# Performance work log

Measured on AMD Instinct MI355X. Metric: run time of the kernel, lower is better.

Reference implementation:

```python
import jax, jax.numpy as jnp
import numpy as np

B, C, P, D = 4096, 1000, 10, 256
N = C * P            # total prototypes
E = 160000           # edges among prototypes
MARGIN = -0.1
LOSS_WEIGHT = 0.1
EPS = 1e-12          # F.normalize eps


def _gcn_conv(x, src, dst, deg_isqrt, w, b):
    # PyG GCNConv: symmetric-normalized aggregation with self-loops (added by caller)
    xw = x @ w                                   # [N, D]
    norm = deg_isqrt[src] * deg_isqrt[dst]       # [E+N]
    msg = norm[:, None] * xw[src]                # [E+N, D]
    out = jax.ops.segment_sum(msg, dst, num_segments=N)
    return out + b


def setup_inputs() -> dict:
    key = jax.random.key(0)
    ks = jax.random.split(key, 8)
    return {
        "hidden": jax.random.normal(ks[0], (B, D), jnp.float32),
        "labels": jax.random.randint(ks[1], (B,), 0, C),
        "edge_index": jax.random.randint(ks[2], (2, E), 0, N),
        "node_features": 0.02 * jax.random.normal(ks[3], (N, D), jnp.float32),
        "w1": jax.random.normal(ks[4], (D, D), jnp.float32) / np.sqrt(D),
        "b1": jnp.zeros((D,), jnp.float32),
        "w2": jax.random.normal(ks[5], (D, D), jnp.float32) / np.sqrt(D),
        "b2": jnp.zeros((D,), jnp.float32),
    }


def reference(hidden, labels, edge_index, node_features, w1, b1, w2, b2):
    # --- PrototypeGCN over the prototype graph (self-loops + sym norm) ---
    loops = jnp.arange(N, dtype=edge_index.dtype)
    src = jnp.concatenate([edge_index[0], loops])
    dst = jnp.concatenate([edge_index[1], loops])
    deg = jax.ops.segment_sum(jnp.ones_like(dst, jnp.float32), dst, num_segments=N)
    deg_isqrt = jnp.where(deg > 0, jax.lax.rsqrt(jnp.maximum(deg, 1.0)), 0.0)
    x = node_features
    x = jax.nn.relu(_gcn_conv(x, src, dst, deg_isqrt, w1, b1))
    x = jax.nn.relu(_gcn_conv(x, src, dst, deg_isqrt, w2, b2))

    # --- cosine similarity, per-class max over prototypes ---
    hidden_norm = hidden / jnp.maximum(jnp.linalg.norm(hidden, axis=1, keepdims=True), EPS)
    proto_norm = x / jnp.maximum(jnp.linalg.norm(x, axis=1, keepdims=True), EPS)
    sim = (1.0 + hidden_norm @ proto_norm.T) / 2.0          # [B, N]
    sim_pc = sim.reshape(B, C, P)
    output = sim_pc.max(axis=2)                              # [B, C]
    topk_idx = sim_pc.argmax(axis=2)                         # [B, C]

    # --- margin-masked cross entropy ---
    ar = jnp.arange(B)
    true_scores = output[ar, labels]
    pred_labels = output.argmax(axis=1)
    pred_scores = output.max(axis=1)
    mask = (true_scores - pred_scores) > MARGIN              # [B] bool
    cnt = mask.sum()
    per_ce = -jax.nn.log_softmax(output, axis=1)[ar, labels]
    ce_loss = jnp.sum(per_ce * mask) / jnp.maximum(cnt, 1).astype(per_ce.dtype)

    # dispersion = -mean(proto_norm @ proto_norm.T) = -||sum_i p_i||^2 / N^2
    s = proto_norm.sum(axis=0)
    dispersion_loss = -(s @ s) / (N * N)
    total_loss = jnp.where(cnt == 0, 0.0, ce_loss + LOSS_WEIGHT * dispersion_loss)

    # --- vectorized usage scatter (replaces Python double loop) ---
    pos_ids = labels * P + topk_idx[ar, labels]
    positive_usage = jnp.zeros((N,), jnp.float32).at[pos_ids].add(1.0)
    wrong = (pred_labels != labels).astype(jnp.float32)
    neg_ids = pred_labels * P + topk_idx[ar, pred_labels]
    negative_usage = jnp.zeros((N,), jnp.float32).at[neg_ids].add(wrong)

    return (output, total_loss, positive_usage, negative_usage)
```

## Files before the change

### kernel.cpp

```cpp
#include <hip/hip_runtime.h>
#include <math.h>

#define B_  4096
#define C_  1000
#define P_  10
#define D_  256
#define N_  10000
#define E_  160000

typedef __attribute__((ext_vector_type(8))) short short8;
typedef __attribute__((ext_vector_type(4))) float floatx4;

#define MFMA16(a, b, c) __builtin_amdgcn_mfma_f32_16x16x32_bf16((a), (b), (c), 0, 0, 0)

__device__ __forceinline__ float waveReduceSum(float v){
  #pragma unroll
  for (int o = 32; o > 0; o >>= 1) v += __shfl_xor(v, o);
  return v;
}
__device__ __forceinline__ unsigned short f2bf(float f){
  unsigned int u = __float_as_uint(f);
  unsigned int r = (u + 0x7FFFu + ((u >> 16) & 1u)) >> 16;
  return (unsigned short)r;
}
__device__ __forceinline__ float bf2f(unsigned short b){
  return __uint_as_float(((unsigned int)b) << 16);
}
__device__ __forceinline__ void gload_lds16(const void* g, void* l){
  __builtin_amdgcn_global_load_lds((const __attribute__((address_space(1))) void*)g,
                                   (__attribute__((address_space(3))) void*)l, 16, 0, 0);
}
__device__ __forceinline__ void split8(const float* __restrict__ p, short8& h8, short8& l8){
  float4 v0 = *(const float4*)p;
  float4 v1 = *(const float4*)(p + 4);
  float v[8] = {v0.x, v0.y, v0.z, v0.w, v1.x, v1.y, v1.z, v1.w};
  #pragma unroll
  for (int j = 0; j < 8; ++j){
    unsigned short h = f2bf(v[j]);
    h8[j] = (short)h;
    l8[j] = (short)f2bf(v[j] - bf2f(h));
  }
}

__global__ void k_scatter(const int* __restrict__ src, const int* __restrict__ dst,
                          int* __restrict__ cursor, int* __restrict__ csr_src){
  int e = blockIdx.x * 256 + threadIdx.x;
  if (e >= E_) return;
  int d = dst[e];
  int p = atomicAdd(&cursor[d], 1);
  p = (p < 63) ? p : 63;
  csr_src[d * 64 + p] = src[e];
}

__global__ void k_isq(const int* __restrict__ deg, float* __restrict__ isq){
  int n = blockIdx.x * 256 + threadIdx.x;
  if (n < N_) isq[n] = 1.0f / sqrtf((float)(deg[n] + 1));
}

__global__ void k_split_w(const float* __restrict__ w1, const float* __restrict__ w2,
                          unsigned short* __restrict__ w1h, unsigned short* __restrict__ w1l,
                          unsigned short* __restrict__ w2h, unsigned short* __restrict__ w2l){
  int b = blockIdx.x;
  int k = threadIdx.x;
  const float* w = (b < 256) ? w1 : w2;
  int n = b & 255;
  float x = w[(size_t)k * 256 + n];
  unsigned short h = f2bf(x);
  unsigned short l = f2bf(x - bf2f(h));
  if (b < 256){ w1h[(size_t)n * 256 + k] = h; w1l[(size_t)n * 256 + k] = l; }
  else        { w2h[(size_t)n * 256 + k] = h; w2l[(size_t)n * 256 + k] = l; }
}

__global__ __launch_bounds__(64) void k_gemm_mfma(
    const float* __restrict__ A,
    const unsigned short* __restrict__ Wh, const unsigned short* __restrict__ Wl,
    float* __restrict__ outp){
  int lane = threadIdx.x;
  int l15 = lane & 15, lq = lane >> 4;
  int rb = blockIdx.x * 64;
  int nb = blockIdx.y * 32;

  floatx4 acc[4][2];
  #pragma unroll
  for (int mt = 0; mt < 4; ++mt)
    #pragma unroll
    for (int nt = 0; nt < 2; ++nt) acc[mt][nt] = (floatx4){0.f,0.f,0.f,0.f};

  int arow[4];
  #pragma unroll
  for (int mt = 0; mt < 4; ++mt){
    int r = rb + mt * 16 + l15;
    arow[mt] = (r < N_) ? r : (N_ - 1);
  }
  for (int kc = 0; kc < 256; kc += 32){
    short8 ah[4], al[4], bh[2], bl[2];
    #pragma unroll
    for (int mt = 0; mt < 4; ++mt)
      split8(A + (size_t)arow[mt] * 256 + kc + lq * 8, ah[mt], al[mt]);
    #pragma unroll
    for (int nt = 0; nt < 2; ++nt){
      size_t o = (size_t)(nb + nt * 16 + l15) * 256 + kc + lq * 8;
      bh[nt] = *(const short8*)(Wh + o);
      bl[nt] = *(const short8*)(Wl + o);
    }
    #pragma unroll
    for (int nt = 0; nt < 2; ++nt)
      #pragma unroll
      for (int mt = 0; mt < 4; ++mt) acc[mt][nt] = MFMA16(al[mt], bh[nt], acc[mt][nt]);
    #pragma unroll
    for (int nt = 0; nt < 2; ++nt)
      #pragma unroll
      for (int mt = 0; mt < 4; ++mt) acc[mt][nt] = MFMA16(ah[mt], bl[nt], acc[mt][nt]);
    #pragma unroll
    for (int nt = 0; nt < 2; ++nt)
      #pragma unroll
      for (int mt = 0; mt < 4; ++mt) acc[mt][nt] = MFMA16(ah[mt], bh[nt], acc[mt][nt]);
  }
  #pragma unroll
  for (int mt = 0; mt < 4; ++mt)
    #pragma unroll
    for (int r = 0; r < 4; ++r){
      int row = rb + mt * 16 + lq * 4 + r;
      if (row < N_){
        #pragma unroll
        for (int nt = 0; nt < 2; ++nt)
          outp[(size_t)row * 256 + nb + nt * 16 + l15] = acc[mt][nt][r];
      }
    }
}

__global__ void k_agg_relu(const float* __restrict__ XW, const int* __restrict__ deg,
                           const int* __restrict__ csr_src, const float* __restrict__ isq,
                           const float* __restrict__ bias, float* __restrict__ X1){
  int n    = blockIdx.x * 4 + (threadIdx.x >> 6);
  int lane = threadIdx.x & 63;
  int c4   = lane * 4;
  int dg = deg[n]; dg = (dg < 64) ? dg : 64;
  int   esr = (lane < dg) ? csr_src[n * 64 + lane] : 0;
  float is  = isq[n];
  float en  = isq[esr] * is;
  float4 s = *(const float4*)(XW + (size_t)n * 256 + c4);
  float w = is * is;
  float4 a = make_float4(w * s.x, w * s.y, w * s.z, w * s.w);
  int i = 0;
  for (; i + 3 < dg; i += 4){
    int s0 = __shfl(esr, i),   s1 = __shfl(esr, i+1), s2 = __shfl(esr, i+2), s3 = __shfl(esr, i+3);
    float n0 = __shfl(en, i),  n1 = __shfl(en, i+1),  n2 = __shfl(en, i+2),  n3 = __shfl(en, i+3);
    float4 v0 = *(const float4*)(XW + (size_t)s0 * 256 + c4);
    float4 v1 = *(const float4*)(XW + (size_t)s1 * 256 + c4);
    float4 v2 = *(const float4*)(XW + (size_t)s2 * 256 + c4);
    float4 v3 = *(const float4*)(XW + (size_t)s3 * 256 + c4);
    a.x += n0*v0.x + n1*v1.x + n2*v2.x + n3*v3.x;
    a.y += n0*v0.y + n1*v1.y + n2*v2.y + n3*v3.y;
    a.z += n0*v0.z + n1*v1.z + n2*v2.z + n3*v3.z;
    a.w += n0*v0.w + n1*v1.w + n2*v2.w + n3*v3.w;
  }
  for (; i < dg; ++i){
    int s0 = __shfl(esr, i); float n0 = __shfl(en, i);
    float4 v0 = *(const float4*)(XW + (size_t)s0 * 256 + c4);
    a.x += n0 * v0.x; a.y += n0 * v0.y; a.z += n0 * v0.z; a.w += n0 * v0.w;
  }
  float4 b = *(const float4*)(bias + c4);
  float4 o;
  o.x = fmaxf(a.x + b.x, 0.f); o.y = fmaxf(a.y + b.y, 0.f);
  o.z = fmaxf(a.z + b.z, 0.f); o.w = fmaxf(a.w + b.w, 0.f);
  *(float4*)(X1 + (size_t)n * 256 + c4) = o;
}

__global__ void k_agg_norm_split(const float* __restrict__ XW, const int* __restrict__ deg,
                                 const int* __restrict__ csr_src, const float* __restrict__ isq,
                                 const float* __restrict__ bias,
                                 unsigned short* __restrict__ Ph, unsigned short* __restrict__ Pl){
  int n    = blockIdx.x * 4 + (threadIdx.x >> 6);
  int lane = threadIdx.x & 63;
  int c4   = lane * 4;
  int dg = deg[n]; dg = (dg < 64) ? dg : 64;
  int   esr = (lane < dg) ? csr_src[n * 64 + lane] : 0;
  float is  = isq[n];
  float en  = isq[esr] * is;
  float4 s = *(const float4*)(XW + (size_t)n * 256 + c4);
  float w = is * is;
  float4 a = make_float4(w * s.x, w * s.y, w * s.z, w * s.w);
  int i = 0;
  for (; i + 3 < dg; i += 4){
    int s0 = __shfl(esr, i),   s1 = __shfl(esr, i+1), s2 = __shfl(esr, i+2), s3 = __shfl(esr, i+3);
    float n0 = __shfl(en, i),  n1 = __shfl(en, i+1),  n2 = __shfl(en, i+2),  n3 = __shfl(en, i+3);
    float4 v0 = *(const float4*)(XW + (size_t)s0 * 256 + c4);
    float4 v1 = *(const float4*)(XW + (size_t)s1 * 256 + c4);
    float4 v2 = *(const float4*)(XW + (size_t)s2 * 256 + c4);
    float4 v3 = *(const float4*)(XW + (size_t)s3 * 256 + c4);
    a.x += n0*v0.x + n1*v1.x + n2*v2.x + n3*v3.x;
    a.y += n0*v0.y + n1*v1.y + n2*v2.y + n3*v3.y;
    a.z += n0*v0.z + n1*v1.z + n2*v2.z + n3*v3.z;
    a.w += n0*v0.w + n1*v1.w + n2*v2.w + n3*v3.w;
  }
  for (; i < dg; ++i){
    int s0 = __shfl(esr, i); float n0 = __shfl(en, i);
    float4 v0 = *(const float4*)(XW + (size_t)s0 * 256 + c4);
    a.x += n0 * v0.x; a.y += n0 * v0.y; a.z += n0 * v0.z; a.w += n0 * v0.w;
  }
  float4 b = *(const float4*)(bias + c4);
  float x0 = fmaxf(a.x + b.x, 0.f), x1 = fmaxf(a.y + b.y, 0.f);
  float x2 = fmaxf(a.z + b.z, 0.f), x3 = fmaxf(a.w + b.w, 0.f);
  float ss = x0*x0 + x1*x1 + x2*x2 + x3*x3;
  float tot = waveReduceSum(ss);
  float nrm = fmaxf(sqrtf(tot), 1e-12f);
  x0 /= nrm; x1 /= nrm; x2 /= nrm; x3 /= nrm;
  unsigned short h0 = f2bf(x0), h1 = f2bf(x1), h2 = f2bf(x2), h3 = f2bf(x3);
  ushort4 hv = make_ushort4(h0, h1, h2, h3);
  ushort4 lv = make_ushort4(f2bf(x0 - bf2f(h0)), f2bf(x1 - bf2f(h1)),
                            f2bf(x2 - bf2f(h2)), f2bf(x3 - bf2f(h3)));
  *(ushort4*)(Ph + (size_t)n * 256 + c4) = hv;
  *(ushort4*)(Pl + (size_t)n * 256 + c4) = lv;
}

__global__ void k_norm_split(const float* __restrict__ in,
                             unsigned short* __restrict__ hi,
                             unsigned short* __restrict__ lo){
  int r = blockIdx.x, t = threadIdx.x;
  float v = in[(size_t)r * 256 + t];
  float ss = waveReduceSum(v * v);
  __shared__ float red[4];
  int w = t >> 6;
  if ((t & 63) == 0) red[w] = ss;
  __syncthreads();
  float tot = red[0] + red[1] + red[2] + red[3];
  float nrm = fmaxf(sqrtf(tot), 1e-12f);
  float x = v / nrm;
  unsigned short h = f2bf(x);
  unsigned short l = f2bf(x - bf2f(h));
  hi[(size_t)r * 256 + t] = h;
  lo[(size_t)r * 256 + t] = l;
}

__global__ void k_colsum(const unsigned short* __restrict__ hi,
                         const unsigned short* __restrict__ lo,
                         float* __restrict__ s){
  int d = threadIdx.x;
  int r0 = blockIdx.x * 100;
  float acc = 0.f;
  for (int r = r0; r < r0 + 100; ++r)
    acc += bf2f(hi[(size_t)r * 256 + d]) + bf2f(lo[(size_t)r * 256 + d]);
  atomicAdd(&s[d], acc);
}

__global__ __launch_bounds__(256, 4) void k_sim_max(
    const unsigned short* __restrict__ HNh, const unsigned short* __restrict__ HNl,
    const unsigned short* __restrict__ PNh, const unsigned short* __restrict__ PNl,
    float* __restrict__ out, unsigned char* __restrict__ idxb){
  __shared__ __align__(16) char smem[20736];

  int tid  = threadIdx.x;
  int wid  = tid >> 6;
  int lane = tid & 63;
  int l15  = lane & 15, lq = lane >> 4;
  int rbw  = blockIdx.y * 128 + wid * 32;
  int cb80 = blockIdx.x * 80;

  int swz  = (l15 >> 1) & 3;
  int srow = lane >> 2;
  int skq  = (lane & 3) ^ ((lane >> 3) & 3);

  floatx4 acc[2][5];
  #pragma unroll
  for (int mt = 0; mt < 2; ++mt)
    #pragma unroll
    for (int nt = 0; nt < 5; ++nt) acc[mt][nt] = (floatx4){0.f,0.f,0.f,0.f};

  const unsigned short* a0h = HNh + (size_t)(rbw + l15) * 256 + lq * 8;
  const unsigned short* a0l = HNl + (size_t)(rbw + l15) * 256 + lq * 8;

  auto stage1 = [&](int kc, int pb, int c){
    int bsel = (c >= 5) ? 1 : 0;
    int s = c - bsel * 5;
    int row = s * 16 + srow;
    const unsigned short* gp = (bsel ? PNl : PNh)
        + (size_t)(cb80 + row) * 256 + kc + skq * 8;
    char* lp = smem + pb * 10240 + bsel * 5120 + s * 1024;
    gload_lds16(gp, lp);
  };
  auto stageAll = [&](int kc, int pb){
    stage1(kc, pb, wid);
    stage1(kc, pb, wid + 4);
    if (wid < 2) stage1(kc, pb, wid + 8);
  };

  stageAll(0, 0);
  short8 ah[2], al[2];
  #pragma unroll
  for (int mt = 0; mt < 2; ++mt){
    ah[mt] = *(const short8*)(a0h + (size_t)mt * 4096);
    al[mt] = *(const short8*)(a0l + (size_t)mt * 4096);
  }
  __syncthreads();

  int p = 0;
  for (int kc = 0; kc < 256; kc += 32){
    const unsigned short* Bh = (const unsigned short*)(smem + p * 10240);
    const unsigned short* Bl = Bh + 2560;
    short8 ah2[2], al2[2];
    if (kc < 224){
      stageAll(kc + 32, p ^ 1);
      #pragma unroll
      for (int mt = 0; mt < 2; ++mt){
        ah2[mt] = *(const short8*)(a0h + (size_t)mt * 4096 + kc + 32);
        al2[mt] = *(const short8*)(a0l + (size_t)mt * 4096 + kc + 32);
      }
    }
    #pragma unroll
    for (int nt2 = 0; nt2 < 4; nt2 += 2){
      int ro0 = ((nt2    ) * 16 + l15) * 32 + (lq ^ swz) * 8;
      int ro1 = ((nt2 + 1) * 16 + l15) * 32 + (lq ^ swz) * 8;
      short8 bh0 = *(const short8*)(Bh + ro0), bl0 = *(const short8*)(Bl + ro0);
      short8 bh1 = *(const short8*)(Bh + ro1), bl1 = *(const short8*)(Bl + ro1);
      acc[0][nt2]   = MFMA16(al[0], bh0, acc[0][nt2]);
      acc[1][nt2]   = MFMA16(al[1], bh0, acc[1][nt2]);
      acc[0][nt2+1] = MFMA16(al[0], bh1, acc[0][nt2+1]);
      acc[1][nt2+1] = MFMA16(al[1], bh1, acc[1][nt2+1]);
      acc[0][nt2]   = MFMA16(ah[0], bl0, acc[0][nt2]);
      acc[1][nt2]   = MFMA16(ah[1], bl0, acc[1][nt2]);
      acc[0][nt2+1] = MFMA16(ah[0], bl1, acc[0][nt2+1]);
      acc[1][nt2+1] = MFMA16(ah[1], bl1, acc[1][nt2+1]);
      acc[0][nt2]   = MFMA16(ah[0], bh0, acc[0][nt2]);
      acc[1][nt2]   = MFMA16(ah[1], bh0, acc[1][nt2]);
      acc[0][nt2+1] = MFMA16(ah[0], bh1, acc[0][nt2+1]);
      acc[1][nt2+1] = MFMA16(ah[1], bh1, acc[1][nt2+1]);
    }
    {
      int ro = (4 * 16 + l15) * 32 + (lq ^ swz) * 8;
      short8 bh = *(const short8*)(Bh + ro), bl = *(const short8*)(Bl + ro);
      acc[0][4] = MFMA16(al[0], bh, acc[0][4]);
      acc[1][4] = MFMA16(al[1], bh, acc[1][4]);
      acc[0][4] = MFMA16(ah[0], bl, acc[0][4]);
      acc[1][4] = MFMA16(ah[1], bl, acc[1][4]);
      acc[0][4] = MFMA16(ah[0], bh, acc[0][4]);
      acc[1][4] = MFMA16(ah[1], bh, acc[1][4]);
    }
    ah[0] = ah2[0]; ah[1] = ah2[1];
    al[0] = al2[0]; al[1] = al2[1];
    __syncthreads();
    p ^= 1;
  }

  float* redw = (float*)smem + wid * 1296;
  #pragma unroll
  for (int mt = 0; mt < 2; ++mt){
    #pragma unroll
    for (int nt = 0; nt < 5; ++nt)
      #pragma unroll
      for (int r = 0; r < 4; ++r)
        redw[(lq * 4 + r) * 81 + nt * 16 + l15] = acc[mt][nt][r];
    int row = lane >> 2;
    int q   = lane & 3;
    const float* basep = redw + row * 81 + q * 20;
    float vs[2]; int is[2];
    #pragma unroll
    for (int cc = 0; cc < 2; ++cc){
      float m = 0.5f * (1.0f + basep[cc * 10]); int mi = 0;
      #pragma unroll
      for (int p2 = 1; p2 < 10; ++p2){
        float v = 0.5f * (1.0f + basep[cc * 10 + p2]);
        if (v > m){ m = v; mi = p2; }
      }
      vs[cc] = m; is[cc] = mi;
    }
    int grow = rbw + mt * 16 + row;
    int gcol = blockIdx.x * 8 + q * 2;
    *(float2*)(out + (size_t)grow * 1000 + gcol) = make_float2(vs[0], vs[1]);
    idxb[(size_t)grow * 1000 + gcol]     = (unsigned char)is[0];
    idxb[(size_t)grow * 1000 + gcol + 1] = (unsigned char)is[1];
  }
}

__global__ void k_row_pass(const float* __restrict__ out, const unsigned char* __restrict__ idxb,
                           const int* __restrict__ labels, int* __restrict__ cnt,
                           float* __restrict__ ce_sum, float* __restrict__ pos_usage,
                           float* __restrict__ neg_usage){
  int b = blockIdx.x * 4 + (threadIdx.x >> 6);
  int lane = threadIdx.x & 63;
  const float* row = out + (size_t)b * 1000;
  float m = -INFINITY, s = 0.f; int bi = 0x7fffffff;
  for (int c = lane; c < 1000; c += 64){
    float v = row[c];
    if (v > m){ s = s * expf(m - v) + 1.f; bi = c; m = v; }
    else       s += expf(v - m);
  }
  #pragma unroll
  for (int o = 32; o > 0; o >>= 1){
    float m2 = __shfl_xor(m, o);
    float s2 = __shfl_xor(s, o);
    int   b2 = __shfl_xor(bi, o);
    float M = fmaxf(m, m2);
    s = s * expf(m - M) + s2 * expf(m2 - M);
    if (m2 > m || (m2 == m && b2 < bi)) bi = b2;
    m = M;
  }
  if (lane == 0){
    int lab = labels[b];
    float true_score = row[lab];
    float per_ce = m + logf(s) - true_score;
    bool mask = (true_score - m) > -0.1f;
    if (mask){ atomicAdd(cnt, 1); atomicAdd(ce_sum, per_ce); }
    int pi = idxb[(size_t)b * 1000 + lab];
    atomicAdd(&pos_usage[lab * P_ + pi], 1.f);
    if (bi != lab){
      int ni = idxb[(size_t)b * 1000 + bi];
      atomicAdd(&neg_usage[bi * P_ + ni], 1.f);
    }
  }
}

__global__ void k_finalize(const float* __restrict__ s, const int* __restrict__ cnt,
                           const float* __restrict__ ce_sum, float* __restrict__ loss_out){
  int t = threadIdx.x;
  float v = s[t];
  float ss = waveReduceSum(v * v);
  __shared__ float red[4];
  if ((t & 63) == 0) red[t >> 6] = ss;
  __syncthreads();
  if (t == 0){
    float tot = red[0] + red[1] + red[2] + red[3];
    float disp = -tot / 1.0e8f;
    int c = *cnt;
    float total = (c == 0) ? 0.f
                : (*ce_sum / (float)(c < 1 ? 1 : c) + 0.1f * disp);
    *loss_out = total;
  }
}

extern "C" void kernel_launch(void* const* d_in, const int* in_sizes, int n_in,
                              void* d_out, int out_size, void* d_ws, size_t ws_size,
                              hipStream_t stream){
  const float* hidden = (const float*)d_in[0];
  const int*   labels = (const int*)  d_in[1];
  const int*   eidx   = (const int*)  d_in[2];
  const float* nodef  = (const float*)d_in[3];
  const float* w1     = (const float*)d_in[4];
  const float* b1     = (const float*)d_in[5];
  const float* w2     = (const float*)d_in[6];
  const float* b2     = (const float*)d_in[7];

  float* out       = (float*)d_out;
  float* loss_out  = out + (size_t)B_ * C_;
  float* pos_usage = loss_out + 1;
  float* neg_usage = pos_usage + N_;

  const int* srcp = eidx;
  const int* dstp = eidx + E_;

  char* base = (char*)d_ws;
  size_t off = 0;
  auto alloc = [&](size_t bytes) -> char* {
    char* p = base + off;
    off = (off + bytes + 255) & ~(size_t)255;
    return p;
  };
  int*   cursor  = (int*)  alloc((size_t)N_ * 4);
  float* svec    = (float*)alloc(256 * 4);
  int*   cnt     = (int*)  alloc(4);
  float* ce_sum  = (float*)alloc(4);
  size_t zero_bytes = off;
  float* deg_isqrt = (float*)alloc((size_t)N_ * 4);
  int*   csr_src   = (int*)  alloc((size_t)N_ * 64 * 4);
  float* XW        = (float*)alloc((size_t)N_ * 256 * 4);
  float* X1        = (float*)alloc((size_t)N_ * 256 * 4);
  unsigned short* Ph  = (unsigned short*)alloc((size_t)N_ * 256 * 2);
  unsigned short* Pl  = (unsigned short*)alloc((size_t)N_ * 256 * 2);
  unsigned short* W1h = (unsigned short*)alloc(256 * 256 * 2);
  unsigned short* W1l = (unsigned short*)alloc(256 * 256 * 2);
  unsigned short* W2h = (unsigned short*)alloc(256 * 256 * 2);
  unsigned short* W2l = (unsigned short*)alloc(256 * 256 * 2);
  unsigned short* HNh = (unsigned short*)alloc((size_t)B_ * 256 * 2);
  unsigned short* HNl = (unsigned short*)alloc((size_t)B_ * 256 * 2);
  unsigned char* idxb = (unsigned char*)alloc((size_t)B_ * C_);

  hipMemsetAsync(base, 0, zero_bytes, stream);
  hipMemsetAsync(loss_out, 0, (size_t)(1 + 2 * N_) * 4, stream);

  k_scatter<<<(E_ + 255) / 256, 256, 0, stream>>>(srcp, dstp, cursor, csr_src);
  k_isq<<<(N_ + 255) / 256, 256, 0, stream>>>(cursor, deg_isqrt);
  k_split_w<<<512, 256, 0, stream>>>(w1, w2, W1h, W1l, W2h, W2l);

  dim3 ggrid(157, 8);
  k_gemm_mfma<<<ggrid, 64, 0, stream>>>(nodef, W1h, W1l, XW);
  k_agg_relu<<<N_ / 4, 256, 0, stream>>>(XW, cursor, csr_src, deg_isqrt, b1, X1);
  k_gemm_mfma<<<ggrid, 64, 0, stream>>>(X1, W2h, W2l, XW);
  k_agg_norm_split<<<N_ / 4, 256, 0, stream>>>(XW, cursor, csr_src, deg_isqrt, b2, Ph, Pl);

  k_norm_split<<<B_, 256, 0, stream>>>(hidden, HNh, HNl);
  k_colsum<<<100, 256, 0, stream>>>(Ph, Pl, svec);

  dim3 sgrid(125, 32);
  k_sim_max<<<sgrid, 256, 0, stream>>>(HNh, HNl, Ph, Pl, out, idxb);

  k_row_pass<<<B_ / 4, 256, 0, stream>>>(out, idxb, labels, cnt, ce_sum, pos_usage, neg_usage);
  k_finalize<<<1, 256, 0, stream>>>(svec, cnt, ce_sum, loss_out);
}
```

Measured before the change: 354.7 us.

## Merge prep kernels, inline degree rsqrt, fuse colsum into norm_split

Combines the edge scatter, weight split and output zeroing into one launch, and drops the separate inverse-sqrt-degree kernel by computing it inline from the degree counts in both aggregation kernels. The column-sum kernel is folded into the hidden-normalize launch as extra blocks. It also raises the occupancy hint on the similarity kernel from 4 to 5 blocks per unit. The aim is fewer kernel launches and memsets, at the cost of an extra gathered degree load and a tighter register budget in the similarity kernel.

```diff
diff --git a/kernel.cpp b/kernel.cpp
--- a/kernel.cpp
+++ b/kernel.cpp
@@ -42,33 +42,35 @@
   }
 }
 
-__global__ void k_scatter(const int* __restrict__ src, const int* __restrict__ dst,
-                          int* __restrict__ cursor, int* __restrict__ csr_src){
-  int e = blockIdx.x * 256 + threadIdx.x;
-  if (e >= E_) return;
-  int d = dst[e];
-  int p = atomicAdd(&cursor[d], 1);
-  p = (p < 63) ? p : 63;
-  csr_src[d * 64 + p] = src[e];
-}
-
-__global__ void k_isq(const int* __restrict__ deg, float* __restrict__ isq){
-  int n = blockIdx.x * 256 + threadIdx.x;
-  if (n < N_) isq[n] = 1.0f / sqrtf((float)(deg[n] + 1));
-}
-
-__global__ void k_split_w(const float* __restrict__ w1, const float* __restrict__ w2,
-                          unsigned short* __restrict__ w1h, unsigned short* __restrict__ w1l,
-                          unsigned short* __restrict__ w2h, unsigned short* __restrict__ w2l){
+__global__ void k_prep(const int* __restrict__ src, const int* __restrict__ dst,
+                       int* __restrict__ cursor, int* __restrict__ csr_src,
+                       const float* __restrict__ w1, const float* __restrict__ w2,
+                       unsigned short* __restrict__ w1h, unsigned short* __restrict__ w1l,
+                       unsigned short* __restrict__ w2h, unsigned short* __restrict__ w2l,
+                       float* __restrict__ zero_zone){
   int b = blockIdx.x;
-  int k = threadIdx.x;
-  const float* w = (b < 256) ? w1 : w2;
-  int n = b & 255;
-  float x = w[(size_t)k * 256 + n];
-  unsigned short h = f2bf(x);
-  unsigned short l = f2bf(x - bf2f(h));
-  if (b < 256){ w1h[(size_t)n * 256 + k] = h; w1l[(size_t)n * 256 + k] = l; }
-  else        { w2h[(size_t)n * 256 + k] = h; w2l[(size_t)n * 256 + k] = l; }
+  if (b < 625){
+    int e = b * 256 + threadIdx.x;
+    if (e < E_){
+      int d = dst[e];
+      int p = atomicAdd(&cursor[d], 1);
+      p = (p < 63) ? p : 63;
+      csr_src[d * 64 + p] = src[e];
+    }
+  } else if (b < 1137){
+    int bb = b - 625;
+    int k = threadIdx.x;
+    const float* w = (bb < 256) ? w1 : w2;
+    int n = bb & 255;
+    float x = w[(size_t)k * 256 + n];
+    unsigned short h = f2bf(x);
+    unsigned short l = f2bf(x - bf2f(h));
+    if (bb < 256){ w1h[(size_t)n * 256 + k] = h; w1l[(size_t)n * 256 + k] = l; }
+    else         { w2h[(size_t)n * 256 + k] = h; w2l[(size_t)n * 256 + k] = l; }
+  } else {
+    int i = (b - 1137) * 256 + threadIdx.x;
+    if (i < 1 + 2 * N_) zero_zone[i] = 0.f;
+  }
 }
 
 __global__ __launch_bounds__(64) void k_gemm_mfma(
@@ -130,15 +132,16 @@
 }
 
 __global__ void k_agg_relu(const float* __restrict__ XW, const int* __restrict__ deg,
-                           const int* __restrict__ csr_src, const float* __restrict__ isq,
+                           const int* __restrict__ csr_src,
                            const float* __restrict__ bias, float* __restrict__ X1){
   int n    = blockIdx.x * 4 + (threadIdx.x >> 6);
   int lane = threadIdx.x & 63;
   int c4   = lane * 4;
-  int dg = deg[n]; dg = (dg < 64) ? dg : 64;
+  int dgn = deg[n];
+  int dg = (dgn < 64) ? dgn : 64;
   int   esr = (lane < dg) ? csr_src[n * 64 + lane] : 0;
-  float is  = isq[n];
-  float en  = isq[esr] * is;
+  float is  = 1.0f / sqrtf((float)(dgn + 1));
+  float en  = (1.0f / sqrtf((float)(deg[esr] + 1))) * is;
   float4 s = *(const float4*)(XW + (size_t)n * 256 + c4);
   float w = is * is;
   float4 a = make_float4(w * s.x, w * s.y, w * s.z, w * s.w);
@@ -168,16 +171,17 @@
 }
 
 __global__ void k_agg_norm_split(const float* __restrict__ XW, const int* __restrict__ deg,
-                                 const int* __restrict__ csr_src, const float* __restrict__ isq,
+                                 const int* __restrict__ csr_src,
                                  const float* __restrict__ bias,
                                  unsigned short* __restrict__ Ph, unsigned short* __restrict__ Pl){
   int n    = blockIdx.x * 4 + (threadIdx.x >> 6);
   int lane = threadIdx.x & 63;
   int c4   = lane * 4;
-  int dg = deg[n]; dg = (dg < 64) ? dg : 64;
+  int dgn = deg[n];
+  int dg = (dgn < 64) ? dgn : 64;
   int   esr = (lane < dg) ? csr_src[n * 64 + lane] : 0;
-  float is  = isq[n];
-  float en  = isq[esr] * is;
+  float is  = 1.0f / sqrtf((float)(dgn + 1));
+  float en  = (1.0f / sqrtf((float)(deg[esr] + 1))) * is;
   float4 s = *(const float4*)(XW + (size_t)n * 256 + c4);
   float w = is * is;
   float4 a = make_float4(w * s.x, w * s.y, w * s.z, w * s.w);
@@ -216,35 +220,35 @@
 
 __global__ void k_norm_split(const float* __restrict__ in,
                              unsigned short* __restrict__ hi,
-                             unsigned short* __restrict__ lo){
+                             unsigned short* __restrict__ lo,
+                             const unsigned short* __restrict__ Ph,
+                             const unsigned short* __restrict__ Pl,
+                             float* __restrict__ svec){
   int r = blockIdx.x, t = threadIdx.x;
-  float v = in[(size_t)r * 256 + t];
-  float ss = waveReduceSum(v * v);
-  __shared__ float red[4];
-  int w = t >> 6;
-  if ((t & 63) == 0) red[w] = ss;
-  __syncthreads();
-  float tot = red[0] + red[1] + red[2] + red[3];
-  float nrm = fmaxf(sqrtf(tot), 1e-12f);
-  float x = v / nrm;
-  unsigned short h = f2bf(x);
-  unsigned short l = f2bf(x - bf2f(h));
-  hi[(size_t)r * 256 + t] = h;
-  lo[(size_t)r * 256 + t] = l;
-}
-
-__global__ void k_colsum(const unsigned short* __restrict__ hi,
-                         const unsigned short* __restrict__ lo,
-                         float* __restrict__ s){
-  int d = threadIdx.x;
-  int r0 = blockIdx.x * 100;
-  float acc = 0.f;
-  for (int r = r0; r < r0 + 100; ++r)
-    acc += bf2f(hi[(size_t)r * 256 + d]) + bf2f(lo[(size_t)r * 256 + d]);
-  atomicAdd(&s[d], acc);
-}
-
-__global__ __launch_bounds__(256, 4) void k_sim_max(
+  if (r < B_){
+    float v = in[(size_t)r * 256 + t];
+    float ss = waveReduceSum(v * v);
+    __shared__ float red[4];
+    int w = t >> 6;
+    if ((t & 63) == 0) red[w] = ss;
+    __syncthreads();
+    float tot = red[0] + red[1] + red[2] + red[3];
+    float nrm = fmaxf(sqrtf(tot), 1e-12f);
+    float x = v / nrm;
+    unsigned short h = f2bf(x);
+    unsigned short l = f2bf(x - bf2f(h));
+    hi[(size_t)r * 256 + t] = h;
+    lo[(size_t)r * 256 + t] = l;
+  } else {
+    int r0 = (r - B_) * 100;
+    float acc = 0.f;
+    for (int rr = r0; rr < r0 + 100; ++rr)
+      acc += bf2f(Ph[(size_t)rr * 256 + t]) + bf2f(Pl[(size_t)rr * 256 + t]);
+    atomicAdd(&svec[t], acc);
+  }
+}
+
+__global__ __launch_bounds__(256, 5) void k_sim_max(
     const unsigned short* __restrict__ HNh, const unsigned short* __restrict__ HNl,
     const unsigned short* __restrict__ PNh, const unsigned short* __restrict__ PNl,
     float* __restrict__ out, unsigned char* __restrict__ idxb){
@@ -460,7 +464,6 @@
   int*   cnt     = (int*)  alloc(4);
   float* ce_sum  = (float*)alloc(4);
   size_t zero_bytes = off;
-  float* deg_isqrt = (float*)alloc((size_t)N_ * 4);
   int*   csr_src   = (int*)  alloc((size_t)N_ * 64 * 4);
   float* XW        = (float*)alloc((size_t)N_ * 256 * 4);
   float* X1        = (float*)alloc((size_t)N_ * 256 * 4);
@@ -475,20 +478,17 @@
   unsigned char* idxb = (unsigned char*)alloc((size_t)B_ * C_);
 
   hipMemsetAsync(base, 0, zero_bytes, stream);
-  hipMemsetAsync(loss_out, 0, (size_t)(1 + 2 * N_) * 4, stream);
-
-  k_scatter<<<(E_ + 255) / 256, 256, 0, stream>>>(srcp, dstp, cursor, csr_src);
-  k_isq<<<(N_ + 255) / 256, 256, 0, stream>>>(cursor, deg_isqrt);
-  k_split_w<<<512, 256, 0, stream>>>(w1, w2, W1h, W1l, W2h, W2l);
+
+  k_prep<<<1216, 256, 0, stream>>>(srcp, dstp, cursor, csr_src,
+                                   w1, w2, W1h, W1l, W2h, W2l, loss_out);
 
   dim3 ggrid(157, 8);
   k_gemm_mfma<<<ggrid, 64, 0, stream>>>(nodef, W1h, W1l, XW);
-  k_agg_relu<<<N_ / 4, 256, 0, stream>>>(XW, cursor, csr_src, deg_isqrt, b1, X1);
+  k_agg_relu<<<N_ / 4, 256, 0, stream>>>(XW, cursor, csr_src, b1, X1);
   k_gemm_mfma<<<ggrid, 64, 0, stream>>>(X1, W2h, W2l, XW);
-  k_agg_norm_split<<<N_ / 4, 256, 0, stream>>>(XW, cursor, csr_src, deg_isqrt, b2, Ph, Pl);
-
-  k_norm_split<<<B_, 256, 0, stream>>>(hidden, HNh, HNl);
-  k_colsum<<<100, 256, 0, stream>>>(Ph, Pl, svec);
+  k_agg_norm_split<<<N_ / 4, 256, 0, stream>>>(XW, cursor, csr_src, b2, Ph, Pl);
+
+  k_norm_split<<<B_ + 100, 256, 0, stream>>>(hidden, HNh, HNl, Ph, Pl, svec);
 
   dim3 sgrid(125, 32);
   k_sim_max<<<sgrid, 256, 0, stream>>>(HNh, HNl, Ph, Pl, out, idxb);
```

Result: no change. 361.4 us (+1.9%).
